# Optimization experiments

Hardware: AMD Instinct MI355X
Metric: run time of the kernel (lower is better)

The kernel has to match this reference:

```python
import jax, jax.numpy as jnp
import numpy as np

B, S, D, H = 2, 2048, 2048, 16
HD = D // H
WHERE_CONST = -10000.0

def setup_inputs() -> dict:
    key = jax.random.key(0)
    k1, k2, k3 = jax.random.split(key, 3)
    x = jax.random.normal(k1, (B, S, D), dtype=jnp.float32)
    attention_mask = jnp.zeros((B, 1, 1, S), dtype=jnp.float32)
    w_qkv = jax.random.normal(k2, (D, 3 * D), dtype=jnp.float32) * (1.0 / np.sqrt(D))
    b_qkv = jnp.zeros((3 * D,), dtype=jnp.float32)
    w_dense = jax.random.normal(k3, (D, D), dtype=jnp.float32) * (1.0 / np.sqrt(D))
    b_dense = jnp.zeros((D,), dtype=jnp.float32)
    return {"x": x, "attention_mask": attention_mask, "w_qkv": w_qkv,
            "b_qkv": b_qkv, "w_dense": w_dense, "b_dense": b_dense}

def reference(x, attention_mask, w_qkv, b_qkv, w_dense, b_dense):
    # fused QKV projection: [B,S,3D]
    qkv = jnp.einsum('bsd,de->bse', x, w_qkv) + b_qkv
    # [B,S,H,3*hd] -> [B,H,S,3*hd]
    qkv = qkv.reshape(B, S, H, 3 * HD).transpose(0, 2, 1, 3)
    q, k, v = jnp.split(qkv, 3, axis=-1)  # each [B,H,S,hd]
    # scores [B,H,S,S], scaled
    scores = jnp.einsum('bhqd,bhkd->bhqk', q, k) / np.sqrt(HD)
    causal = jnp.tril(jnp.ones((S, S), dtype=bool))[None, None]
    scores = jnp.where(causal, scores, WHERE_CONST)
    scores = scores + attention_mask
    probs = jax.nn.softmax(scores, axis=-1)
    # attention dropout is identity in eval mode
    ctx = jnp.einsum('bhqk,bhkd->bhqd', probs, v)  # [B,H,S,hd]
    ctx = ctx.transpose(0, 2, 1, 3).reshape(B, S, D)
    out = jnp.einsum('bsd,de->bse', ctx, w_dense) + b_dense
    # output dropout is identity in eval mode
    return out
```

## Files before the change

### kernel.cpp

```cpp
#include <hip/hip_runtime.h>
#include <hip/hip_bf16.h>

typedef __bf16 bf16x8 __attribute__((ext_vector_type(8)));
typedef float f32x4 __attribute__((ext_vector_type(4)));
typedef float f32x16 __attribute__((ext_vector_type(16)));
typedef unsigned short u16;

#define S_ 2048
#define D_ 2048
#define H_ 16
#define HD_ 128
#define SCALE_ 0.08838834764831845f

__device__ __forceinline__ u16 f2bf(float f) {
  unsigned u = __builtin_bit_cast(unsigned, f);
  u += 0x7fffu + ((u >> 16) & 1u);
  return (u16)(u >> 16);
}

__device__ __forceinline__ void gload16(void* lds, const void* g) {
  __builtin_amdgcn_global_load_lds((const __attribute__((address_space(1))) void*)g,
                                   (__attribute__((address_space(3))) void*)lds, 16, 0, 0);
}

__device__ __forceinline__ f32x4 mfma16(bf16x8 a, bf16x8 b, f32x4 c) {
  return __builtin_amdgcn_mfma_f32_16x16x32_bf16(a, b, c, 0, 0, 0);
}
__device__ __forceinline__ f32x16 mfma32(bf16x8 a, bf16x8 b, f32x16 c) {
  return __builtin_amdgcn_mfma_f32_32x32x16_bf16(a, b, c, 0, 0, 0);
}

__device__ __forceinline__ unsigned cvt_pk_bf16(float lo, float hi) {
  unsigned r;
  asm("v_cvt_pk_bf16_f32 %0, %1, %2" : "=v"(r) : "v"(lo), "v"(hi));
  return r;
}

__global__ void k_cast_bf16(const float* __restrict__ in, u16* __restrict__ out, int n4) {
  int i = blockIdx.x * blockDim.x + threadIdx.x;
  if (i < n4) {
    float4 v = ((const float4*)in)[i];
    ushort4 o;
    o.x = f2bf(v.x); o.y = f2bf(v.y); o.z = f2bf(v.z); o.w = f2bf(v.w);
    ((ushort4*)out)[i] = o;
  }
}

__global__ void k_transpose_cast(const float* __restrict__ in, u16* __restrict__ out,
                                 int rows, int cols) {
  __shared__ u16 tile[32][33];
  int c0 = blockIdx.x * 32, r0 = blockIdx.y * 32;
  int tx = threadIdx.x, ty = threadIdx.y;
#pragma unroll
  for (int i = 0; i < 4; i++) {
    int r = r0 + ty + i * 8;
    tile[ty + i * 8][tx] = f2bf(in[(long)r * cols + c0 + tx]);
  }
  __syncthreads();
#pragma unroll
  for (int i = 0; i < 4; i++) {
    int c = c0 + ty + i * 8;
    out[(long)c * rows + r0 + tx] = tile[tx][ty + i * 8];
  }
}

__global__ void k_extract_vt(const u16* __restrict__ qkv, u16* __restrict__ vt) {
  __shared__ u16 tile[32][33];
  int bh = blockIdx.z, b = bh >> 4, h = bh & 15;
  int d0 = blockIdx.x * 32, s0 = blockIdx.y * 32;
  int tx = threadIdx.x, ty = threadIdx.y;
#pragma unroll
  for (int i = 0; i < 4; i++) {
    int s = s0 + ty + i * 8;
    tile[ty + i * 8][tx] = qkv[(long)(b * S_ + s) * 6144 + h * 384 + 256 + d0 + tx];
  }
  __syncthreads();
#pragma unroll
  for (int i = 0; i < 4; i++) {
    int d = d0 + ty + i * 8;
    vt[((long)bh * HD_ + d) * S_ + s0 + tx] = tile[tx][ty + i * 8];
  }
}

template <bool BF16OUT>
__global__ __launch_bounds__(512) void k_gemm2(const u16* __restrict__ A,
                                               const u16* __restrict__ Bt,
                                               const float* __restrict__ bias,
                                               void* __restrict__ Cv,
                                               int M, int N, int K, int NTM) {
  __shared__ __align__(16) u16 lA[2][256 * 64];
  __shared__ __align__(16) u16 lB[2][128 * 64];
  const int tid = threadIdx.x, w = tid >> 6, l = tid & 63;
  const int wr = w >> 1, wc = w & 1, lr = l & 15, lg = l >> 4;
  const int nwg = NTM * (N >> 7);
  const int per = nwg >> 3;
  const int wgid = ((int)blockIdx.x & 7) * per + ((int)blockIdx.x >> 3);
  const int tm = (wgid % NTM) << 8;
  const int tn = (wgid / NTM) << 7;
  const int NT = K >> 6;

  f32x4 acc[4][4];
#pragma unroll
  for (int m = 0; m < 4; m++)
#pragma unroll
    for (int n = 0; n < 4; n++) acc[m][n] = {0.f, 0.f, 0.f, 0.f};

  auto stageA = [&](int buf, int kt) {
#pragma unroll
    for (int i = 0; i < 4; i++) {
      int base = i * 512 + w * 64;
      int fl = base + l, r = fl >> 3, cg = (fl & 7) ^ (r & 7);
      gload16(&lA[buf][base * 8], &A[(long)(tm + r) * K + kt * 64 + cg * 8]);
    }
  };
  auto stageB = [&](int buf, int kt) {
#pragma unroll
    for (int i = 0; i < 2; i++) {
      int base = i * 512 + w * 64;
      int fl = base + l, r = fl >> 3, cg = (fl & 7) ^ (r & 7);
      gload16(&lB[buf][base * 8], &Bt[(long)(tn + r) * K + kt * 64 + cg * 8]);
    }
  };

  stageA(0, 0);
  stageB(0, 0);
  if (NT > 1) stageA(1, 1);
  asm volatile("s_waitcnt vmcnt(4)" ::: "memory");
  __builtin_amdgcn_s_barrier();

  for (int kt = 0; kt < NT; ++kt) {
    const int b = kt & 1;
    bf16x8 af[4][2], bfr[2][2];
#pragma unroll
    for (int m = 0; m < 4; m++)
#pragma unroll
      for (int k = 0; k < 2; k++) {
        int r = wr * 64 + m * 16 + lr;
        af[m][k] = *(const bf16x8*)&lA[b][r * 64 + ((((k << 2) + lg) ^ (r & 7)) << 3)];
      }
#pragma unroll
    for (int n = 0; n < 2; n++)
#pragma unroll
      for (int k = 0; k < 2; k++) {
        int r = wc * 64 + n * 16 + lr;
        bfr[n][k] = *(const bf16x8*)&lB[b][r * 64 + ((((k << 2) + lg) ^ (r & 7)) << 3)];
      }
    if (kt + 1 < NT) stageB(b ^ 1, kt + 1);
    __builtin_amdgcn_s_barrier();
    asm volatile("s_waitcnt lgkmcnt(0)" ::: "memory");
    __builtin_amdgcn_sched_barrier(0);
    __builtin_amdgcn_s_setprio(1);
#pragma unroll
    for (int m = 0; m < 4; m++)
#pragma unroll
      for (int n = 0; n < 2; n++)
#pragma unroll
        for (int k = 0; k < 2; k++)
          acc[m][n] = mfma16(af[m][k], bfr[n][k], acc[m][n]);
    __builtin_amdgcn_s_setprio(0);
    __builtin_amdgcn_s_barrier();

#pragma unroll
    for (int n = 0; n < 2; n++)
#pragma unroll
      for (int k = 0; k < 2; k++) {
        int r = wc * 64 + (n + 2) * 16 + lr;
        bfr[n][k] = *(const bf16x8*)&lB[b][r * 64 + ((((k << 2) + lg) ^ (r & 7)) << 3)];
      }
    if (kt + 2 < NT) stageA(b, kt + 2);
    __builtin_amdgcn_s_barrier();
    if (kt + 2 < NT)
      asm volatile("s_waitcnt vmcnt(4) lgkmcnt(0)" ::: "memory");
    else
      asm volatile("s_waitcnt vmcnt(0) lgkmcnt(0)" ::: "memory");
    __builtin_amdgcn_sched_barrier(0);
    __builtin_amdgcn_s_setprio(1);
#pragma unroll
    for (int m = 0; m < 4; m++)
#pragma unroll
      for (int n = 0; n < 2; n++)
#pragma unroll
        for (int k = 0; k < 2; k++)
          acc[m][n + 2] = mfma16(af[m][k], bfr[n][k], acc[m][n + 2]);
    __builtin_amdgcn_s_setprio(0);
    __builtin_amdgcn_s_barrier();
  }

#pragma unroll
  for (int n = 0; n < 4; n++) {
    int col = tn + wc * 64 + n * 16 + lr;
    float bv = bias[col];
#pragma unroll
    for (int m = 0; m < 4; m++) {
      int row0 = tm + wr * 64 + m * 16 + lg * 4;
#pragma unroll
      for (int j = 0; j < 4; j++) {
        float v = acc[m][n][j] + bv;
        if constexpr (BF16OUT)
          ((u16*)Cv)[(long)(row0 + j) * N + col] = f2bf(v);
        else
          ((float*)Cv)[(long)(row0 + j) * N + col] = v;
      }
    }
  }
}

__global__ __launch_bounds__(256) void k_attn(const u16* __restrict__ qkv,
                                              const u16* __restrict__ vt,
                                              const float* __restrict__ amask,
                                              u16* __restrict__ ctx) {
  __shared__ u16 lK[2][64 * 128];
  __shared__ u16 lV[2][128 * 64];
  __shared__ float lAM[S_];
  const int bh = blockIdx.x, b = bh >> 4, h = bh & 15;
  const int c = blockIdx.y;
  const int tid = threadIdx.x, w = tid >> 6, l = tid & 63;
  const int lr5 = l & 31, hi = l >> 5;
  const int qrow0 = (w < 2) ? (c * 64 + w * 32) : ((31 - c) * 64 + (w - 2) * 32);
  const int ntiles = 32 - c;

  for (int i = tid; i < S_; i += 256) lAM[i] = amask[b * S_ + i];

  bf16x8 qf[8];
#pragma unroll
  for (int ks = 0; ks < 8; ks++)
    qf[ks] = *(const bf16x8*)&qkv[(long)(b * S_ + qrow0 + lr5) * 6144 +
                                  h * 384 + ks * 16 + hi * 8];

  f32x16 aO[4];
#pragma unroll
  for (int db = 0; db < 4; db++)
#pragma unroll
    for (int r = 0; r < 16; r++) aO[db][r] = 0.f;
  float mrun = -3.0e38f, lrun = 0.f;

  auto stage = [&](int buf, int t) {
#pragma unroll
    for (int i = 0; i < 4; i++) {
      int base = i * 256 + w * 64;
      int f = base + l;
      int r = f >> 4, cg = (f & 15) ^ (r & 7);
      gload16(&lK[buf][base * 8],
              &qkv[(long)(b * S_ + t * 64 + r) * 6144 + h * 384 + 128 + cg * 8]);
    }
#pragma unroll
    for (int i = 0; i < 4; i++) {
      int base = i * 256 + w * 64;
      int f = base + l;
      int r = f >> 3, cg = (f & 7) ^ (r & 7);
      gload16(&lV[buf][base * 8], &vt[((long)bh * HD_ + r) * S_ + t * 64 + cg * 8]);
    }
  };

  stage(0, 0);
  __syncthreads();

  for (int t = 0; t < ntiles; ++t) {
    const int cur = t & 1;
    if (t + 1 < ntiles) stage(cur ^ 1, t + 1);

    if (t * 64 <= qrow0 + 31) {
      const int t64 = t * 64;
      const int qr = qrow0 + lr5;
      f32x16 aS0, aS1;
#pragma unroll
      for (int r = 0; r < 16; r++) { aS0[r] = 0.f; aS1[r] = 0.f; }
      __builtin_amdgcn_s_setprio(1);
#pragma unroll
      for (int ks = 0; ks < 8; ks++) {
        int cg = 2 * ks + hi;
        bf16x8 kf0 = *(const bf16x8*)&lK[cur][lr5 * 128 + ((cg ^ (lr5 & 7)) << 3)];
        bf16x8 kf1 = *(const bf16x8*)&lK[cur][(32 + lr5) * 128 + ((cg ^ (lr5 & 7)) << 3)];
        aS0 = mfma32(kf0, qf[ks], aS0);
        aS1 = mfma32(kf1, qf[ks], aS1);
      }
      __builtin_amdgcn_s_setprio(0);

      float v0[16], v1[16];
      const bool needmask = (t64 + 63 > qrow0);
#pragma unroll
      for (int rg = 0; rg < 4; rg++) {
        f32x4 am0 = *(const f32x4*)&lAM[t64 + rg * 8 + hi * 4];
        f32x4 am1 = *(const f32x4*)&lAM[t64 + 32 + rg * 8 + hi * 4];
#pragma unroll
        for (int j = 0; j < 4; j++) {
          v0[rg * 4 + j] = fmaf(aS0[rg * 4 + j], SCALE_, am0[j]);
          v1[rg * 4 + j] = fmaf(aS1[rg * 4 + j], SCALE_, am1[j]);
          if (needmask) {
            if (t64 + rg * 8 + 4 * hi + j > qr)      v0[rg * 4 + j] = -1e30f;
            if (t64 + 32 + rg * 8 + 4 * hi + j > qr) v1[rg * 4 + j] = -1e30f;
          }
        }
      }
      float mx = v0[0];
#pragma unroll
      for (int i = 1; i < 16; i++) mx = fmaxf(mx, v0[i]);
#pragma unroll
      for (int i = 0; i < 16; i++) mx = fmaxf(mx, v1[i]);
      mx = fmaxf(mx, __shfl_xor(mx, 32));

      if (!__all(mx <= mrun + 8.0f)) {
        float mnew = fmaxf(mrun, mx);
        float corr = __expf(mrun - mnew);
        lrun *= corr;
        mrun = mnew;
#pragma unroll
        for (int reg = 0; reg < 16; reg++) {
          float cb = __shfl(corr, (reg & 3) + 8 * (reg >> 2) + 4 * hi);
#pragma unroll
          for (int db = 0; db < 4; db++) aO[db][reg] *= cb;
        }
      }

      float p0[16], p1[16], ls = 0.f;
#pragma unroll
      for (int i = 0; i < 16; i++) { p0[i] = __expf(v0[i] - mrun); ls += p0[i]; }
#pragma unroll
      for (int i = 0; i < 16; i++) { p1[i] = __expf(v1[i] - mrun); ls += p1[i]; }
      ls += __shfl_xor(ls, 32);
      lrun += ls;

      unsigned pk0[8], pk1[8];
#pragma unroll
      for (int q = 0; q < 8; q++) {
        pk0[q] = cvt_pk_bf16(p0[2 * q], p0[2 * q + 1]);
        pk1[q] = cvt_pk_bf16(p1[2 * q], p1[2 * q + 1]);
      }
      bf16x8 pa[4];
#pragma unroll
      for (int kst = 0; kst < 4; kst++) {
        const int j4 = kst & 1;
        unsigned a0, a1, a2, a3;
        if (kst < 2) { a0 = pk0[4 * j4]; a1 = pk0[4 * j4 + 1]; a2 = pk0[4 * j4 + 2]; a3 = pk0[4 * j4 + 3]; }
        else         { a0 = pk1[4 * j4]; a1 = pk1[4 * j4 + 1]; a2 = pk1[4 * j4 + 2]; a3 = pk1[4 * j4 + 3]; }
        unsigned s0 = hi ? a0 : a2;
        unsigned s1 = hi ? a1 : a3;
        unsigned r0 = __shfl_xor(s0, 32);
        unsigned r1 = __shfl_xor(s1, 32);
        union { unsigned u[4]; bf16x8 v; } U;
        U.u[0] = hi ? r0 : a0;
        U.u[1] = hi ? r1 : a1;
        U.u[2] = hi ? a2 : r0;
        U.u[3] = hi ? a3 : r1;
        pa[kst] = U.v;
      }

      __builtin_amdgcn_s_setprio(1);
#pragma unroll
      for (int kst = 0; kst < 4; kst++) {
#pragma unroll
        for (int db = 0; db < 4; db++) {
          int d = db * 32 + lr5;
          int cg = (2 * kst + hi) ^ (d & 7);
          bf16x8 vb = *(const bf16x8*)&lV[cur][d * 64 + (cg << 3)];
          aO[db] = mfma32(pa[kst], vb, aO[db]);
        }
      }
      __builtin_amdgcn_s_setprio(0);
    }
    __syncthreads();
  }

  float inv = 1.0f / lrun;
#pragma unroll
  for (int reg = 0; reg < 16; reg++) {
    int r = (reg & 3) + 8 * (reg >> 2) + 4 * hi;
    float ib = __shfl(inv, r);
    int srow = qrow0 + r;
#pragma unroll
    for (int db = 0; db < 4; db++)
      ctx[(long)(b * S_ + srow) * D_ + h * HD_ + db * 32 + lr5] = f2bf(aO[db][reg] * ib);
  }
}

extern "C" void kernel_launch(void* const* d_in, const int* in_sizes, int n_in,
                              void* d_out, int out_size, void* d_ws, size_t ws_size,
                              hipStream_t stream) {
  const float* x  = (const float*)d_in[0];
  const float* am = (const float*)d_in[1];
  const float* wq = (const float*)d_in[2];
  const float* bq = (const float*)d_in[3];
  const float* wd = (const float*)d_in[4];
  const float* bd = (const float*)d_in[5];
  float* out = (float*)d_out;
  char* ws = (char*)d_ws;

  u16* xb   = (u16*)(ws);
  u16* wqT  = (u16*)(ws + (size_t)16777216);
  u16* qkvb = (u16*)(ws + (size_t)41943040);
  u16* vtb  = (u16*)(ws + (size_t)16777216);
  u16* wdT  = (u16*)(ws + (size_t)33554432);
  u16* ctxb = (u16*)(ws);

  k_cast_bf16<<<8192, 256, 0, stream>>>(x, xb, 2097152);
  k_transpose_cast<<<dim3(192, 64), dim3(32, 8), 0, stream>>>(wq, wqT, 2048, 6144);
  k_gemm2<true><<<768, 512, 0, stream>>>(xb, wqT, bq, (void*)qkvb, 4096, 6144, 2048, 16);
  k_extract_vt<<<dim3(4, 64, 32), dim3(32, 8), 0, stream>>>(qkvb, vtb);
  k_transpose_cast<<<dim3(64, 64), dim3(32, 8), 0, stream>>>(wd, wdT, 2048, 2048);
  k_attn<<<dim3(32, 16), 256, 0, stream>>>(qkvb, vtb, am, ctxb);
  k_gemm2<false><<<256, 512, 0, stream>>>(ctxb, wdT, bd, (void*)out, 4096, 2048, 2048, 16);
}
```

Measured before the change: 312.7 us.

## Load attention K/V tiles directly from global memory into registers, dropping LDS staging

The attention kernel no longer stages K and V tiles through double-buffered LDS with block-wide barriers. Each wave now loads its K, V and mask fragments straight from global memory into registers and runs only as many tiles as its own causal extent needs. This removes the LDS traffic, the __syncthreads per tile and the waits on the slowest wave, and declares two blocks per CU in launch bounds. The cost is that K/V data shared across waves is no longer reused, so each wave re-reads it through the caches, and register pressure rises with the 16 V fragments held per tile.

After: 322.9 us. 1.03x slower.

```diff
diff --git a/kernel.cpp b/kernel.cpp
--- a/kernel.cpp
+++ b/kernel.cpp
@@ -205,27 +205,23 @@
   }
 }
 
-__global__ __launch_bounds__(256) void k_attn(const u16* __restrict__ qkv,
-                                              const u16* __restrict__ vt,
-                                              const float* __restrict__ amask,
-                                              u16* __restrict__ ctx) {
-  __shared__ u16 lK[2][64 * 128];
-  __shared__ u16 lV[2][128 * 64];
-  __shared__ float lAM[S_];
+__global__ __launch_bounds__(256, 2) void k_attn(const u16* __restrict__ qkv,
+                                                 const u16* __restrict__ vt,
+                                                 const float* __restrict__ amask,
+                                                 u16* __restrict__ ctx) {
   const int bh = blockIdx.x, b = bh >> 4, h = bh & 15;
-  const int c = blockIdx.y;
+  const int pr = blockIdx.y;
   const int tid = threadIdx.x, w = tid >> 6, l = tid & 63;
   const int lr5 = l & 31, hi = l >> 5;
-  const int qrow0 = (w < 2) ? (c * 64 + w * 32) : ((31 - c) * 64 + (w - 2) * 32);
-  const int ntiles = 32 - c;
-
-  for (int i = tid; i < S_; i += 256) lAM[i] = amask[b * S_ + i];
+  const int qrow0 = (w < 2) ? (pr * 64 + w * 32) : ((31 - pr) * 64 + (w - 2) * 32);
+  const int nt = (qrow0 >> 6) + 1;
 
   bf16x8 qf[8];
-#pragma unroll
-  for (int ks = 0; ks < 8; ks++)
-    qf[ks] = *(const bf16x8*)&qkv[(long)(b * S_ + qrow0 + lr5) * 6144 +
-                                  h * 384 + ks * 16 + hi * 8];
+  {
+    const u16* qp = qkv + (long)(b * S_ + qrow0 + lr5) * 6144 + h * 384 + hi * 8;
+#pragma unroll
+    for (int ks = 0; ks < 8; ks++) qf[ks] = *(const bf16x8*)(qp + ks * 16);
+  }
 
   f32x16 aO[4];
 #pragma unroll
@@ -234,131 +230,121 @@
     for (int r = 0; r < 16; r++) aO[db][r] = 0.f;
   float mrun = -3.0e38f, lrun = 0.f;
 
-  auto stage = [&](int buf, int t) {
-#pragma unroll
-    for (int i = 0; i < 4; i++) {
-      int base = i * 256 + w * 64;
-      int f = base + l;
-      int r = f >> 4, cg = (f & 15) ^ (r & 7);
-      gload16(&lK[buf][base * 8],
-              &qkv[(long)(b * S_ + t * 64 + r) * 6144 + h * 384 + 128 + cg * 8]);
-    }
-#pragma unroll
-    for (int i = 0; i < 4; i++) {
-      int base = i * 256 + w * 64;
-      int f = base + l;
-      int r = f >> 3, cg = (f & 7) ^ (r & 7);
-      gload16(&lV[buf][base * 8], &vt[((long)bh * HD_ + r) * S_ + t * 64 + cg * 8]);
-    }
-  };
-
-  stage(0, 0);
-  __syncthreads();
-
-  for (int t = 0; t < ntiles; ++t) {
-    const int cur = t & 1;
-    if (t + 1 < ntiles) stage(cur ^ 1, t + 1);
-
-    if (t * 64 <= qrow0 + 31) {
-      const int t64 = t * 64;
-      const int qr = qrow0 + lr5;
-      f32x16 aS0, aS1;
-#pragma unroll
-      for (int r = 0; r < 16; r++) { aS0[r] = 0.f; aS1[r] = 0.f; }
-      __builtin_amdgcn_s_setprio(1);
-#pragma unroll
-      for (int ks = 0; ks < 8; ks++) {
-        int cg = 2 * ks + hi;
-        bf16x8 kf0 = *(const bf16x8*)&lK[cur][lr5 * 128 + ((cg ^ (lr5 & 7)) << 3)];
-        bf16x8 kf1 = *(const bf16x8*)&lK[cur][(32 + lr5) * 128 + ((cg ^ (lr5 & 7)) << 3)];
-        aS0 = mfma32(kf0, qf[ks], aS0);
-        aS1 = mfma32(kf1, qf[ks], aS1);
-      }
-      __builtin_amdgcn_s_setprio(0);
-
-      float v0[16], v1[16];
-      const bool needmask = (t64 + 63 > qrow0);
-#pragma unroll
-      for (int rg = 0; rg < 4; rg++) {
-        f32x4 am0 = *(const f32x4*)&lAM[t64 + rg * 8 + hi * 4];
-        f32x4 am1 = *(const f32x4*)&lAM[t64 + 32 + rg * 8 + hi * 4];
-#pragma unroll
-        for (int j = 0; j < 4; j++) {
-          v0[rg * 4 + j] = fmaf(aS0[rg * 4 + j], SCALE_, am0[j]);
-          v1[rg * 4 + j] = fmaf(aS1[rg * 4 + j], SCALE_, am1[j]);
-          if (needmask) {
-            if (t64 + rg * 8 + 4 * hi + j > qr)      v0[rg * 4 + j] = -1e30f;
-            if (t64 + 32 + rg * 8 + 4 * hi + j > qr) v1[rg * 4 + j] = -1e30f;
-          }
+  const u16* kb0 = qkv + (long)b * S_ * 6144 + h * 384 + 128 + hi * 8;
+  const u16* vb0 = vt + (long)bh * HD_ * S_ + hi * 8;
+  const float* ab0 = amask + b * S_;
+
+  for (int t = 0; t < nt; ++t) {
+    const int t64 = t << 6;
+    const int qr = qrow0 + lr5;
+
+    const u16* kr0 = kb0 + (long)(t64 + lr5) * 6144;
+    const u16* kr1 = kr0 + 32 * 6144;
+    bf16x8 kf0[8], kf1[8];
+#pragma unroll
+    for (int ks = 0; ks < 8; ks++) kf0[ks] = *(const bf16x8*)(kr0 + ks * 16);
+#pragma unroll
+    for (int ks = 0; ks < 8; ks++) kf1[ks] = *(const bf16x8*)(kr1 + ks * 16);
+
+    f32x16 aS0, aS1;
+#pragma unroll
+    for (int r = 0; r < 16; r++) { aS0[r] = 0.f; aS1[r] = 0.f; }
+    __builtin_amdgcn_s_setprio(1);
+#pragma unroll
+    for (int ks = 0; ks < 8; ks++) {
+      aS0 = mfma32(kf0[ks], qf[ks], aS0);
+      aS1 = mfma32(kf1[ks], qf[ks], aS1);
+    }
+    __builtin_amdgcn_s_setprio(0);
+
+    bf16x8 vbf[16];
+#pragma unroll
+    for (int kst = 0; kst < 4; kst++)
+#pragma unroll
+      for (int db = 0; db < 4; db++)
+        vbf[kst * 4 + db] =
+            *(const bf16x8*)(vb0 + (long)(db * 32 + lr5) * S_ + t64 + kst * 16);
+    f32x4 am0[4], am1[4];
+#pragma unroll
+    for (int rg = 0; rg < 4; rg++) {
+      am0[rg] = *(const f32x4*)(ab0 + t64 + rg * 8 + hi * 4);
+      am1[rg] = *(const f32x4*)(ab0 + t64 + 32 + rg * 8 + hi * 4);
+    }
+
+    float v0[16], v1[16];
+    const bool needmask = (t64 + 63 > qrow0);
+#pragma unroll
+    for (int rg = 0; rg < 4; rg++) {
+#pragma unroll
+      for (int j = 0; j < 4; j++) {
+        v0[rg * 4 + j] = fmaf(aS0[rg * 4 + j], SCALE_, am0[rg][j]);
+        v1[rg * 4 + j] = fmaf(aS1[rg * 4 + j], SCALE_, am1[rg][j]);
+        if (needmask) {
+          if (t64 + rg * 8 + 4 * hi + j > qr)      v0[rg * 4 + j] = -1e30f;
+          if (t64 + 32 + rg * 8 + 4 * hi + j > qr) v1[rg * 4 + j] = -1e30f;
         }
       }
-      float mx = v0[0];
-#pragma unroll
-      for (int i = 1; i < 16; i++) mx = fmaxf(mx, v0[i]);
-#pragma unroll
-      for (int i = 0; i < 16; i++) mx = fmaxf(mx, v1[i]);
-      mx = fmaxf(mx, __shfl_xor(mx, 32));
-
-      if (!__all(mx <= mrun + 8.0f)) {
-        float mnew = fmaxf(mrun, mx);
-        float corr = __expf(mrun - mnew);
-        lrun *= corr;
-        mrun = mnew;
-#pragma unroll
-        for (int reg = 0; reg < 16; reg++) {
-          float cb = __shfl(corr, (reg & 3) + 8 * (reg >> 2) + 4 * hi);
-#pragma unroll
-          for (int db = 0; db < 4; db++) aO[db][reg] *= cb;
-        }
-      }
-
-      float p0[16], p1[16], ls = 0.f;
-#pragma unroll
-      for (int i = 0; i < 16; i++) { p0[i] = __expf(v0[i] - mrun); ls += p0[i]; }
-#pragma unroll
-      for (int i = 0; i < 16; i++) { p1[i] = __expf(v1[i] - mrun); ls += p1[i]; }
-      ls += __shfl_xor(ls, 32);
-      lrun += ls;
-
-      unsigned pk0[8], pk1[8];
-#pragma unroll
-      for (int q = 0; q < 8; q++) {
-        pk0[q] = cvt_pk_bf16(p0[2 * q], p0[2 * q + 1]);
-        pk1[q] = cvt_pk_bf16(p1[2 * q], p1[2 * q + 1]);
-      }
-      bf16x8 pa[4];
-#pragma unroll
-      for (int kst = 0; kst < 4; kst++) {
-        const int j4 = kst & 1;
-        unsigned a0, a1, a2, a3;
-        if (kst < 2) { a0 = pk0[4 * j4]; a1 = pk0[4 * j4 + 1]; a2 = pk0[4 * j4 + 2]; a3 = pk0[4 * j4 + 3]; }
-        else         { a0 = pk1[4 * j4]; a1 = pk1[4 * j4 + 1]; a2 = pk1[4 * j4 + 2]; a3 = pk1[4 * j4 + 3]; }
-        unsigned s0 = hi ? a0 : a2;
-        unsigned s1 = hi ? a1 : a3;
-        unsigned r0 = __shfl_xor(s0, 32);
-        unsigned r1 = __shfl_xor(s1, 32);
-        union { unsigned u[4]; bf16x8 v; } U;
-        U.u[0] = hi ? r0 : a0;
-        U.u[1] = hi ? r1 : a1;
-        U.u[2] = hi ? a2 : r0;
-        U.u[3] = hi ? a3 : r1;
-        pa[kst] = U.v;
-      }
-
-      __builtin_amdgcn_s_setprio(1);
-#pragma unroll
-      for (int kst = 0; kst < 4; kst++) {
-#pragma unroll
-        for (int db = 0; db < 4; db++) {
-          int d = db * 32 + lr5;
-          int cg = (2 * kst + hi) ^ (d & 7);
-          bf16x8 vb = *(const bf16x8*)&lV[cur][d * 64 + (cg << 3)];
-          aO[db] = mfma32(pa[kst], vb, aO[db]);
-        }
-      }
-      __builtin_amdgcn_s_setprio(0);
-    }
-    __syncthreads();
+    }
+    float mx = v0[0];
+#pragma unroll
+    for (int i = 1; i < 16; i++) mx = fmaxf(mx, v0[i]);
+#pragma unroll
+    for (int i = 0; i < 16; i++) mx = fmaxf(mx, v1[i]);
+    mx = fmaxf(mx, __shfl_xor(mx, 32));
+
+    if (!__all(mx <= mrun + 8.0f)) {
+      float mnew = fmaxf(mrun, mx);
+      float corr = __expf(mrun - mnew);
+      lrun *= corr;
+      mrun = mnew;
+#pragma unroll
+      for (int reg = 0; reg < 16; reg++) {
+        float cb = __shfl(corr, (reg & 3) + 8 * (reg >> 2) + 4 * hi);
+#pragma unroll
+        for (int db = 0; db < 4; db++) aO[db][reg] *= cb;
+      }
+    }
+
+    float p0[16], p1[16], ls = 0.f;
+#pragma unroll
+    for (int i = 0; i < 16; i++) { p0[i] = __expf(v0[i] - mrun); ls += p0[i]; }
+#pragma unroll
+    for (int i = 0; i < 16; i++) { p1[i] = __expf(v1[i] - mrun); ls += p1[i]; }
+    ls += __shfl_xor(ls, 32);
+    lrun += ls;
+
+    unsigned pk0[8], pk1[8];
+#pragma unroll
+    for (int q = 0; q < 8; q++) {
+      pk0[q] = cvt_pk_bf16(p0[2 * q], p0[2 * q + 1]);
+      pk1[q] = cvt_pk_bf16(p1[2 * q], p1[2 * q + 1]);
+    }
+    bf16x8 pa[4];
+#pragma unroll
+    for (int kst = 0; kst < 4; kst++) {
+      const int j4 = kst & 1;
+      unsigned a0, a1, a2, a3;
+      if (kst < 2) { a0 = pk0[4 * j4]; a1 = pk0[4 * j4 + 1]; a2 = pk0[4 * j4 + 2]; a3 = pk0[4 * j4 + 3]; }
+      else         { a0 = pk1[4 * j4]; a1 = pk1[4 * j4 + 1]; a2 = pk1[4 * j4 + 2]; a3 = pk1[4 * j4 + 3]; }
+      unsigned s0 = hi ? a0 : a2;
+      unsigned s1 = hi ? a1 : a3;
+      unsigned r0 = __shfl_xor(s0, 32);
+      unsigned r1 = __shfl_xor(s1, 32);
+      union { unsigned u[4]; bf16x8 v; } U;
+      U.u[0] = hi ? r0 : a0;
+      U.u[1] = hi ? r1 : a1;
+      U.u[2] = hi ? a2 : r0;
+      U.u[3] = hi ? a3 : r1;
+      pa[kst] = U.v;
+    }
+
+    __builtin_amdgcn_s_setprio(1);
+#pragma unroll
+    for (int kst = 0; kst < 4; kst++)
+#pragma unroll
+      for (int db = 0; db < 4; db++)
+        aO[db] = mfma32(pa[kst], vbf[kst * 4 + db], aO[db]);
+    __builtin_amdgcn_s_setprio(0);
   }
 
   float inv = 1.0f / lrun;
```
